# Kernel optimization log

Hardware: AMD Instinct MI355X
Metric: run time of the kernel (lower is better)

## Reference

```python
import jax, jax.numpy as jnp
import numpy as np

N = 100000          # nodes
E = 1600000         # edges (before self-loops)
F_IN = 128          # raw node features
TOPO = 8            # topological feature dim
HEADS1, HID1 = 8, 8 # conv1: 8 heads x 8 channels, concat -> 64
C_OUT = 40          # classes (conv2: 1 head, no concat)
NEG_SLOPE = 0.2     # PyG GATConv leaky_relu slope


def setup_inputs() -> dict:
    key = jax.random.key(0)
    ks = jax.random.split(key, 12)
    x = jax.random.normal(ks[0], (N, F_IN), jnp.float32)
    topo = jax.random.normal(ks[1], (N, TOPO), jnp.float32)
    edge_index = jax.random.randint(ks[2], (2, E), 0, N, jnp.int32)
    s = 0.1
    W1 = jax.random.normal(ks[3], (F_IN + TOPO, HEADS1 * HID1), jnp.float32) * s
    a_src1 = jax.random.normal(ks[4], (HEADS1, HID1), jnp.float32) * s
    a_dst1 = jax.random.normal(ks[5], (HEADS1, HID1), jnp.float32) * s
    b1 = jnp.zeros((HEADS1 * HID1,), jnp.float32)
    W2 = jax.random.normal(ks[6], (HEADS1 * HID1, C_OUT), jnp.float32) * s
    a_src2 = jax.random.normal(ks[7], (1, C_OUT), jnp.float32) * s
    a_dst2 = jax.random.normal(ks[8], (1, C_OUT), jnp.float32) * s
    b2 = jnp.zeros((C_OUT,), jnp.float32)
    return {"x": x, "topo": topo, "edge_index": edge_index,
            "W1": W1, "a_src1": a_src1, "a_dst1": a_dst1, "b1": b1,
            "W2": W2, "a_src2": a_src2, "a_dst2": a_dst2, "b2": b2}


def _gat_conv(x, src, dst, W, a_src, a_dst, b, heads, concat):
    # x: [N, Fin]; src/dst: [Etot] (self-loops already included)
    n = x.shape[0]
    h = (x @ W).reshape(n, heads, -1)                 # [N, H, C]
    alpha_s = jnp.sum(h * a_src[None], axis=-1)       # [N, H]
    alpha_d = jnp.sum(h * a_dst[None], axis=-1)       # [N, H]
    e = jax.nn.leaky_relu(alpha_s[src] + alpha_d[dst], NEG_SLOPE)  # [Etot, H]
    # segment softmax over destination nodes (numerically stable)
    m = jax.ops.segment_max(e, dst, num_segments=n)   # [N, H]
    ex = jnp.exp(e - m[dst])
    z = jax.ops.segment_sum(ex, dst, num_segments=n)  # [N, H]
    alpha = ex / (z[dst] + 1e-16)                     # [Etot, H]
    out = jax.ops.segment_sum(h[src] * alpha[..., None], dst, num_segments=n)  # [N,H,C]
    out = out.reshape(n, -1) if concat else out.mean(axis=1)
    return out + b


def reference(x, topo, edge_index, W1, a_src1, a_dst1, b1, W2, a_src2, a_dst2, b2):
    n = x.shape[0]
    loops = jnp.arange(n, dtype=edge_index.dtype)
    src = jnp.concatenate([edge_index[0], loops])  # PyG add_self_loops=True
    dst = jnp.concatenate([edge_index[1], loops])
    h = jnp.concatenate([x, topo], axis=1)         # [N, F_IN + TOPO]
    # dropout is identity in eval mode
    h = jax.nn.elu(_gat_conv(h, src, dst, W1, a_src1, a_dst1, b1, HEADS1, True))
    logits = _gat_conv(h, src, dst, W2, a_src2, a_dst2, b2, 1, False)
    return jax.nn.log_softmax(logits, axis=1)
```

## Files before the change

### kernel.cpp

```cpp
#include <hip/hip_runtime.h>
#include <math.h>


#define NBUK_MAX 512
#define BIN_CHUNK 4096
#define BUK_CAP 4608

typedef unsigned short ushort_t;

__device__ inline unsigned int f2bf(float f) {
    unsigned int u = __float_as_uint(f);
    u += 0x7FFFu + ((u >> 16) & 1u);
    return u >> 16;
}
__device__ inline float bf_lo(unsigned int u) {
    return __uint_as_float(u << 16);
}
__device__ inline float bf_hi(unsigned int u) {
    return __uint_as_float(u & 0xFFFF0000u);
}
__device__ inline float lrelu_exp(float q) {
    return __expf(q >= 0.f ? q : 0.2f * q);
}

__device__ inline int wave_incl_scan(int v, int lane) {
    #pragma unroll
    for (int ofs = 1; ofs < 64; ofs <<= 1) {
        int t = __shfl_up(v, ofs);
        if (lane >= ofs) v += t;
    }
    return v;
}

__global__ __launch_bounds__(256) void k_bin(const int* __restrict__ src,
                                             const int* __restrict__ dst,
                                             int* __restrict__ gCursor,
                                             unsigned int* __restrict__ tmp,
                                             int E, int NBUK) {
    __shared__ int lcnt[NBUK_MAX];
    __shared__ int lcur[NBUK_MAX];
    int tid = threadIdx.x;
    int base = blockIdx.x * BIN_CHUNK;
    for (int i = tid; i < NBUK; i += 256) lcnt[i] = 0;
    __syncthreads();
    int d[16];
    #pragma unroll
    for (int q = 0; q < 4; q++) {
        int e = base + q * 1024 + 4 * tid;
        if (e + 3 < E) {
            int4 v = *(const int4*)&dst[e];
            d[4 * q + 0] = v.x; d[4 * q + 1] = v.y;
            d[4 * q + 2] = v.z; d[4 * q + 3] = v.w;
        } else {
            #pragma unroll
            for (int k = 0; k < 4; k++)
                d[4 * q + k] = (e + k < E) ? dst[e + k] : -1;
        }
    }
    #pragma unroll
    for (int k = 0; k < 16; k++)
        if (d[k] >= 0) atomicAdd(&lcnt[d[k] >> 8], 1);
    __syncthreads();
    for (int b = tid; b < NBUK; b += 256) {
        int c = lcnt[b];
        lcur[b] = c ? b * BUK_CAP + atomicAdd(&gCursor[b], c) : 0;
    }
    __syncthreads();
    #pragma unroll
    for (int q = 0; q < 4; q++) {
        int e = base + q * 1024 + 4 * tid;
        int s[4];
        if (e + 3 < E) {
            int4 v = *(const int4*)&src[e];
            s[0] = v.x; s[1] = v.y; s[2] = v.z; s[3] = v.w;
        } else {
            #pragma unroll
            for (int k = 0; k < 4; k++)
                s[k] = (e + k < E) ? src[e + k] : 0;
        }
        #pragma unroll
        for (int k = 0; k < 4; k++) {
            int dd = d[4 * q + k];
            if (dd >= 0) {
                int p = atomicAdd(&lcur[dd >> 8], 1);
                tmp[p] = ((unsigned int)s[k] << 8) | (unsigned int)(dd & 255);
            }
        }
    }
}

__global__ __launch_bounds__(512) void k_fill2(const unsigned int* __restrict__ tmp,
                                               const int* __restrict__ gCursor,
                                               int* __restrict__ rowptr,
                                               int* __restrict__ rowEnd,
                                               int* __restrict__ csr, int N) {
    __shared__ int cnt[256];
    __shared__ int cur[256];
    __shared__ int wsum[4];
    int b = blockIdx.x, tid = threadIdx.x;
    int e0 = b * BUK_CAP;
    int cnt_e = gCursor[b];
    int e1 = e0 + cnt_e;
    if (tid < 256) cnt[tid] = 0;
    __syncthreads();
    {
        int nq = cnt_e >> 2;
        const uint4* t4 = (const uint4*)(tmp + e0);
        for (int q = tid; q < nq; q += 512) {
            uint4 v = t4[q];
            atomicAdd(&cnt[v.x & 255u], 1);
            atomicAdd(&cnt[v.y & 255u], 1);
            atomicAdd(&cnt[v.z & 255u], 1);
            atomicAdd(&cnt[v.w & 255u], 1);
        }
        for (int i = (nq << 2) + tid; i < cnt_e; i += 512)
            atomicAdd(&cnt[tmp[e0 + i] & 255u], 1);
    }
    __syncthreads();
    if (tid < 256) {
        int lane = tid & 63, wv = tid >> 6;
        int v = cnt[tid];
        int incl = wave_incl_scan(v, lane);
        if (lane == 63) wsum[wv] = incl;
        cnt[tid] = incl - v;
    }
    __syncthreads();
    if (tid < 256) {
        int wv = tid >> 6;
        int woff = 0;
        for (int i = 0; i < wv; i++) woff += wsum[i];
        int excl = woff + cnt[tid];
        int node = b * 256 + tid;
        int start = e0 + excl;
        cur[tid] = start;
        if (node < N) {
            rowptr[node] = start;
        }
    }
    __syncthreads();
    if (tid < 256) {
        int node = b * 256 + tid;
        if (node < N) rowEnd[node] = (tid < 255) ? cur[tid + 1] : e1;
    }
    __syncthreads();
    for (int i = e0 + tid; i < e1; i += 512) {
        unsigned int t = tmp[i];
        int p = atomicAdd(&cur[t & 255u], 1);
        csr[p] = (int)(t >> 8);
    }
}

__global__ __launch_bounds__(256) void k_xform1(const float* __restrict__ x,
                                                const float* __restrict__ topo,
                                                const float* __restrict__ W1,
                                                const float* __restrict__ asrc,
                                                const float* __restrict__ adst,
                                                ushort_t* __restrict__ h1b,
                                                float* __restrict__ as1,
                                                float* __restrict__ ad1, int N) {
    __shared__ float XT[136 * 64];
    __shared__ float WS[136 * 64];
    int tid = threadIdx.x;
    int n0 = blockIdx.x * 64;
    {
        const float4* W4 = (const float4*)W1;
        float4* WS4 = (float4*)WS;
        for (int i = tid; i < 2176; i += 256) WS4[i] = W4[i];
    }
    {
        const float4* x4 = (const float4*)x;
        for (int i = tid; i < 2048; i += 256) {
            int node = i & 63, k4 = i >> 6;
            int gn = n0 + node; if (gn > N - 1) gn = N - 1;
            float4 v = x4[(size_t)gn * 32 + k4];
            int k = k4 * 4;
            XT[(k + 0) * 64 + node] = v.x;
            XT[(k + 1) * 64 + node] = v.y;
            XT[(k + 2) * 64 + node] = v.z;
            XT[(k + 3) * 64 + node] = v.w;
        }
        const float4* t4 = (const float4*)topo;
        if (tid < 128) {
            int node = tid & 63, j4 = tid >> 6;
            int gn = n0 + node; if (gn > N - 1) gn = N - 1;
            float4 v = t4[(size_t)gn * 2 + j4];
            int k = 128 + j4 * 4;
            XT[(k + 0) * 64 + node] = v.x;
            XT[(k + 1) * 64 + node] = v.y;
            XT[(k + 2) * 64 + node] = v.z;
            XT[(k + 3) * 64 + node] = v.w;
        }
    }
    __syncthreads();
    int ci = tid & 15, ni = tid >> 4;
    int nb = ni * 4, cb = ci * 4;
    float acc[16];
    #pragma unroll
    for (int i = 0; i < 16; i++) acc[i] = 0.f;
    #pragma unroll 4
    for (int k = 0; k < 136; k++) {
        float4 xv = *(const float4*)&XT[k * 64 + nb];
        float4 wv = *(const float4*)&WS[k * 64 + cb];
        acc[0]  = fmaf(xv.x, wv.x, acc[0]);  acc[1]  = fmaf(xv.x, wv.y, acc[1]);
        acc[2]  = fmaf(xv.x, wv.z, acc[2]);  acc[3]  = fmaf(xv.x, wv.w, acc[3]);
        acc[4]  = fmaf(xv.y, wv.x, acc[4]);  acc[5]  = fmaf(xv.y, wv.y, acc[5]);
        acc[6]  = fmaf(xv.y, wv.z, acc[6]);  acc[7]  = fmaf(xv.y, wv.w, acc[7]);
        acc[8]  = fmaf(xv.z, wv.x, acc[8]);  acc[9]  = fmaf(xv.z, wv.y, acc[9]);
        acc[10] = fmaf(xv.z, wv.z, acc[10]); acc[11] = fmaf(xv.z, wv.w, acc[11]);
        acc[12] = fmaf(xv.w, wv.x, acc[12]); acc[13] = fmaf(xv.w, wv.y, acc[13]);
        acc[14] = fmaf(xv.w, wv.z, acc[14]); acc[15] = fmaf(xv.w, wv.w, acc[15]);
    }
    int head = cb >> 3;
    #pragma unroll
    for (int i = 0; i < 4; i++) {
        int n = n0 + nb + i;
        unsigned int p0 = f2bf(acc[i * 4 + 0]) | (f2bf(acc[i * 4 + 1]) << 16);
        unsigned int p1 = f2bf(acc[i * 4 + 2]) | (f2bf(acc[i * 4 + 3]) << 16);
        if (n < N) *(uint2*)&h1b[(size_t)n * 64 + cb] = make_uint2(p0, p1);
        float s = 0.f, d = 0.f;
        #pragma unroll
        for (int j = 0; j < 4; j++) {
            s = fmaf(acc[i * 4 + j], asrc[cb + j], s);
            d = fmaf(acc[i * 4 + j], adst[cb + j], d);
        }
        s += __shfl_xor(s, 1);
        d += __shfl_xor(d, 1);
        if ((ci & 1) == 0 && n < N) {
            as1[n * 8 + head] = s;
            ad1[n * 8 + head] = d;
        }
    }
}

#define AGG_FMA(W_, U_)                                           \
    {                                                             \
        acc[0] = fmaf(W_, bf_lo(U_.x), acc[0]);                   \
        acc[1] = fmaf(W_, bf_hi(U_.x), acc[1]);                   \
        acc[2] = fmaf(W_, bf_lo(U_.y), acc[2]);                   \
        acc[3] = fmaf(W_, bf_hi(U_.y), acc[3]);                   \
        acc[4] = fmaf(W_, bf_lo(U_.z), acc[4]);                   \
        acc[5] = fmaf(W_, bf_hi(U_.z), acc[5]);                   \
        acc[6] = fmaf(W_, bf_lo(U_.w), acc[6]);                   \
        acc[7] = fmaf(W_, bf_hi(U_.w), acc[7]);                   \
        z += W_;                                                  \
    }

#define AGG1_C3(B_)                                                        \
    {                                                                      \
        int e0 = (B_) * 8 + g, e1 = e0 + 8, e2 = e0 + 16;                  \
        int se0 = __shfl(cv, e0 < d ? e0 : dm1);                           \
        int se1 = __shfl(cv, e1 < d ? e1 : dm1);                           \
        int se2 = __shfl(cv, e2 < d ? e2 : dm1);                           \
        float av0 = as1[se0 * 8 + head];                                   \
        float av1 = as1[se1 * 8 + head];                                   \
        float av2 = as1[se2 * 8 + head];                                   \
        uint4 u0 = *(const uint4*)(h1c + (((unsigned)se0 << 7) + hoff));   \
        uint4 u1 = *(const uint4*)(h1c + (((unsigned)se1 << 7) + hoff));   \
        uint4 u2 = *(const uint4*)(h1c + (((unsigned)se2 << 7) + hoff));   \
        float w0 = e0 < d ? lrelu_exp(av0 + adv) : 0.f;                    \
        float w1 = e1 < d ? lrelu_exp(av1 + adv) : 0.f;                    \
        float w2 = e2 < d ? lrelu_exp(av2 + adv) : 0.f;                    \
        AGG_FMA(w0, u0);                                                   \
        AGG_FMA(w1, u1);                                                   \
        AGG_FMA(w2, u2);                                                   \
    }

__global__ __launch_bounds__(256) void k_agg1(const ushort_t* __restrict__ h1b,
                                              const float* __restrict__ as1,
                                              const float* __restrict__ ad1,
                                              const float* __restrict__ b1,
                                              const int* __restrict__ rowptr,
                                              const int* __restrict__ rowEnd,
                                              const int* __restrict__ csr,
                                              float* __restrict__ h2, int N) {
    int tid = threadIdx.x, lane = tid & 63;
    int n = blockIdx.x * 4 + (tid >> 6);
    if (n >= N) return;
    int g = lane >> 3;
    int head = lane & 7;
    const char* h1c = (const char*)h1b;
    unsigned hoff = (unsigned)head << 4;
    float adv = ad1[n * 8 + head];
    float acc[8];
    #pragma unroll
    for (int k = 0; k < 8; k++) acc[k] = 0.f;
    float z = 0.f;

    int j0 = rowptr[n], j1 = rowEnd[n];
    int d = j1 - j0;
    int dm1 = d > 0 ? d - 1 : 0;
    int cv = (d > 0) ? csr[j0 + (lane < d ? lane : dm1)] : 0;

    {
        float w = lrelu_exp(as1[n * 8 + head] + adv);
        if (g == 0) {
            uint4 u = *(const uint4*)(h1c + (((unsigned)n << 7) + hoff));
            acc[0] = w * bf_lo(u.x); acc[1] = w * bf_hi(u.x);
            acc[2] = w * bf_lo(u.y); acc[3] = w * bf_hi(u.y);
            acc[4] = w * bf_lo(u.z); acc[5] = w * bf_hi(u.z);
            acc[6] = w * bf_lo(u.w); acc[7] = w * bf_hi(u.w);
            z = w;
        }
    }
    if (d > 0) {
        AGG1_C3(0);
        if (d > 24) {
            AGG1_C3(3);
            if (d > 48) {
                int e0 = 48 + g, e1 = 56 + g;
                int se0 = __shfl(cv, e0 < d ? e0 : dm1);
                int se1 = __shfl(cv, e1 < d ? e1 : dm1);
                float av0 = as1[se0 * 8 + head];
                float av1 = as1[se1 * 8 + head];
                uint4 u0 = *(const uint4*)(h1c + (((unsigned)se0 << 7) + hoff));
                uint4 u1 = *(const uint4*)(h1c + (((unsigned)se1 << 7) + hoff));
                float w0 = e0 < d ? lrelu_exp(av0 + adv) : 0.f;
                float w1 = e1 < d ? lrelu_exp(av1 + adv) : 0.f;
                AGG_FMA(w0, u0);
                AGG_FMA(w1, u1);
                for (int j = j0 + 64; j < j1; j += 8) {
                    int m = j1 - j;
                    int idx = (lane & 7); idx = idx < m ? idx : m - 1;
                    int cvt = csr[j + idx];
                    int ge = g < m ? g : m - 1;
                    int se = __shfl(cvt, ge);
                    float av = as1[se * 8 + head];
                    uint4 u = *(const uint4*)(h1c + (((unsigned)se << 7) + hoff));
                    float w = (g < m) ? lrelu_exp(av + adv) : 0.f;
                    AGG_FMA(w, u);
                }
            }
        }
    }
    #pragma unroll
    for (int k = 0; k < 8; k++) {
        acc[k] += __shfl_xor(acc[k], 8);
        acc[k] += __shfl_xor(acc[k], 16);
        acc[k] += __shfl_xor(acc[k], 32);
    }
    z += __shfl_xor(z, 8); z += __shfl_xor(z, 16); z += __shfl_xor(z, 32);
    if (g == 0) {
        float inv = 1.f / (z + 1e-16f);
        float o[8];
        #pragma unroll
        for (int k = 0; k < 8; k++) {
            float v = acc[k] * inv + b1[head * 8 + k];
            o[k] = v > 0.f ? v : (__expf(v) - 1.f);
        }
        float4* dp = (float4*)&h2[(size_t)n * 64 + head * 8];
        dp[0] = make_float4(o[0], o[1], o[2], o[3]);
        dp[1] = make_float4(o[4], o[5], o[6], o[7]);
    }
}

__global__ __launch_bounds__(256) void k_xform2(const float* __restrict__ h2,
                                                const float* __restrict__ W2,
                                                const float* __restrict__ asrc2,
                                                const float* __restrict__ adst2,
                                                ushort_t* __restrict__ gb,
                                                float* __restrict__ as2,
                                                float* __restrict__ ad2, int N) {
    __shared__ float XT[64 * 64];
    __shared__ float WS[64 * 40];
    int tid = threadIdx.x;
    int n0 = blockIdx.x * 64;
    {
        const float4* W4 = (const float4*)W2;
        float4* WS4 = (float4*)WS;
        for (int i = tid; i < 640; i += 256) WS4[i] = W4[i];
    }
    {
        const float4* h4 = (const float4*)h2;
        for (int i = tid; i < 1024; i += 256) {
            int node = i & 63, k4 = i >> 6;
            int gn = n0 + node; if (gn > N - 1) gn = N - 1;
            float4 v = h4[(size_t)gn * 16 + k4];
            int k = k4 * 4;
            XT[(k + 0) * 64 + node] = v.x;
            XT[(k + 1) * 64 + node] = v.y;
            XT[(k + 2) * 64 + node] = v.z;
            XT[(k + 3) * 64 + node] = v.w;
        }
    }
    __syncthreads();
    int ci = tid & 15, ni = tid >> 4;
    int nb = ni * 4, cb = ci * 4;
    float acc[16];
    #pragma unroll
    for (int i = 0; i < 16; i++) acc[i] = 0.f;
    if (ci < 10) {
        #pragma unroll 4
        for (int k = 0; k < 64; k++) {
            float4 xv = *(const float4*)&XT[k * 64 + nb];
            float4 wv = *(const float4*)&WS[k * 40 + cb];
            acc[0]  = fmaf(xv.x, wv.x, acc[0]);  acc[1]  = fmaf(xv.x, wv.y, acc[1]);
            acc[2]  = fmaf(xv.x, wv.z, acc[2]);  acc[3]  = fmaf(xv.x, wv.w, acc[3]);
            acc[4]  = fmaf(xv.y, wv.x, acc[4]);  acc[5]  = fmaf(xv.y, wv.y, acc[5]);
            acc[6]  = fmaf(xv.y, wv.z, acc[6]);  acc[7]  = fmaf(xv.y, wv.w, acc[7]);
            acc[8]  = fmaf(xv.z, wv.x, acc[8]);  acc[9]  = fmaf(xv.z, wv.y, acc[9]);
            acc[10] = fmaf(xv.z, wv.z, acc[10]); acc[11] = fmaf(xv.z, wv.w, acc[11]);
            acc[12] = fmaf(xv.w, wv.x, acc[12]); acc[13] = fmaf(xv.w, wv.y, acc[13]);
            acc[14] = fmaf(xv.w, wv.z, acc[14]); acc[15] = fmaf(xv.w, wv.w, acc[15]);
        }
    }
    #pragma unroll
    for (int i = 0; i < 4; i++) {
        int n = n0 + nb + i;
        if (ci < 10 && n < N) {
            unsigned int p0 = f2bf(acc[i * 4 + 0]) | (f2bf(acc[i * 4 + 1]) << 16);
            unsigned int p1 = f2bf(acc[i * 4 + 2]) | (f2bf(acc[i * 4 + 3]) << 16);
            *(uint2*)&gb[(size_t)n * 40 + cb] = make_uint2(p0, p1);
        }
        float s = 0.f, d = 0.f;
        if (ci < 10) {
            #pragma unroll
            for (int j = 0; j < 4; j++) {
                s = fmaf(acc[i * 4 + j], asrc2[cb + j], s);
                d = fmaf(acc[i * 4 + j], adst2[cb + j], d);
            }
        }
        s += __shfl_xor(s, 1); s += __shfl_xor(s, 2);
        s += __shfl_xor(s, 4); s += __shfl_xor(s, 8);
        d += __shfl_xor(d, 1); d += __shfl_xor(d, 2);
        d += __shfl_xor(d, 4); d += __shfl_xor(d, 8);
        if (ci == 0 && n < N) { as2[n] = s; ad2[n] = d; }
    }
}

#define AGG2_C2(B_)                                                            \
    {                                                                          \
        int ew0 = (B_) * 12 + lm12, ew1 = ew0 + 12;                            \
        int sw0 = __shfl(cv, ew0 < d ? ew0 : dm1);                             \
        int sw1 = __shfl(cv, ew1 < d ? ew1 : dm1);                             \
        float av0 = as2[sw0];                                                  \
        float av1 = as2[sw1];                                                  \
        int e00 = (B_) * 12 + gi0, e01 = (B_) * 12 + gi1;                      \
        int e02 = (B_) * 12 + gi2, e03 = (B_) * 12 + gi3;                      \
        int s00 = __shfl(cv, e00 < d ? e00 : dm1);                             \
        int s01 = __shfl(cv, e01 < d ? e01 : dm1);                             \
        int s02 = __shfl(cv, e02 < d ? e02 : dm1);                             \
        int s03 = __shfl(cv, e03 < d ? e03 : dm1);                             \
        int s10 = __shfl(cv, e00 + 12 < d ? e00 + 12 : dm1);                   \
        int s11 = __shfl(cv, e01 + 12 < d ? e01 + 12 : dm1);                   \
        int s12 = __shfl(cv, e02 + 12 < d ? e02 + 12 : dm1);                   \
        int s13 = __shfl(cv, e03 + 12 < d ? e03 + 12 : dm1);                   \
        unsigned int u00 = *(const unsigned int*)(gbc + ((unsigned)s00 * 80u + coff)); \
        unsigned int u01 = *(const unsigned int*)(gbc + ((unsigned)s01 * 80u + coff)); \
        unsigned int u02 = *(const unsigned int*)(gbc + ((unsigned)s02 * 80u + coff)); \
        unsigned int u03 = *(const unsigned int*)(gbc + ((unsigned)s03 * 80u + coff)); \
        unsigned int u10 = *(const unsigned int*)(gbc + ((unsigned)s10 * 80u + coff)); \
        unsigned int u11 = *(const unsigned int*)(gbc + ((unsigned)s11 * 80u + coff)); \
        unsigned int u12 = *(const unsigned int*)(gbc + ((unsigned)s12 * 80u + coff)); \
        unsigned int u13 = *(const unsigned int*)(gbc + ((unsigned)s13 * 80u + coff)); \
        float wall0 = (ew0 < d) ? lrelu_exp(av0 + add) : 0.f;                  \
        float wall1 = (ew1 < d) ? lrelu_exp(av1 + add) : 0.f;                  \
        float w00 = __shfl(wall0, gi0), w01 = __shfl(wall0, gi1);              \
        float w02 = __shfl(wall0, gi2), w03 = __shfl(wall0, gi3);              \
        float w10 = __shfl(wall1, gi0), w11 = __shfl(wall1, gi1);              \
        float w12 = __shfl(wall1, gi2), w13 = __shfl(wall1, gi3);              \
        acc0 = fmaf(w00, bf_lo(u00), acc0); acc1 = fmaf(w00, bf_hi(u00), acc1); zl += w00; \
        acc0 = fmaf(w01, bf_lo(u01), acc0); acc1 = fmaf(w01, bf_hi(u01), acc1); zl += w01; \
        acc0 = fmaf(w02, bf_lo(u02), acc0); acc1 = fmaf(w02, bf_hi(u02), acc1); zl += w02; \
        acc0 = fmaf(w03, bf_lo(u03), acc0); acc1 = fmaf(w03, bf_hi(u03), acc1); zl += w03; \
        acc0 = fmaf(w10, bf_lo(u10), acc0); acc1 = fmaf(w10, bf_hi(u10), acc1); zl += w10; \
        acc0 = fmaf(w11, bf_lo(u11), acc0); acc1 = fmaf(w11, bf_hi(u11), acc1); zl += w11; \
        acc0 = fmaf(w12, bf_lo(u12), acc0); acc1 = fmaf(w12, bf_hi(u12), acc1); zl += w12; \
        acc0 = fmaf(w13, bf_lo(u13), acc0); acc1 = fmaf(w13, bf_hi(u13), acc1); zl += w13; \
    }

__global__ __launch_bounds__(256) void k_agg2(const ushort_t* __restrict__ gb,
                                              const float* __restrict__ as2,
                                              const float* __restrict__ ad2,
                                              const float* __restrict__ b2,
                                              const int* __restrict__ rowptr,
                                              const int* __restrict__ rowEnd,
                                              const int* __restrict__ csr,
                                              float* __restrict__ out, int N) {
    int tid = threadIdx.x, lane = tid & 63;
    int n = blockIdx.x * 4 + (tid >> 6);
    if (n >= N) return;
    int g = lane / 20, p = lane % 20;
    int c0 = 2 * p;
    const char* gbc = (const char*)gb;
    unsigned coff = (unsigned)(p << 2);
    int lm12 = lane % 12;
    int gi0 = (0 + g) < 12 ? (0 + g) : 11;
    int gi1 = (3 + g) < 12 ? (3 + g) : 11;
    int gi2 = (6 + g) < 12 ? (6 + g) : 11;
    int gi3 = (9 + g) < 12 ? (9 + g) : 11;
    float add = ad2[n];
    float acc0 = 0.f, acc1 = 0.f, zl = 0.f;

    int j0 = rowptr[n], j1 = rowEnd[n];
    int d = j1 - j0;
    int dm1 = d > 0 ? d - 1 : 0;
    int cv = (d > 0) ? csr[j0 + (lane < d ? lane : dm1)] : 0;

    {
        float e0 = as2[n] + add;
        float w = lrelu_exp(e0);
        if (g == 0) {
            unsigned int u = *(const unsigned int*)(gbc + ((unsigned)n * 80u + coff));
            acc0 = w * bf_lo(u); acc1 = w * bf_hi(u); zl = w;
        }
    }
    if (d > 0) {
        AGG2_C2(0);
        if (d > 24) {
            AGG2_C2(2);
            if (d > 48) {
                for (int j = j0 + 48; j < j1; j += 12) {
                    int m = j1 - j;
                    int idx = lm12 < m ? lm12 : m - 1;
                    int cvt = csr[j + idx];
                    float av = as2[cvt];
                    float wall = (lm12 < m) ? lrelu_exp(av + add) : 0.f;
                    #pragma unroll
                    for (int i = 0; i < 4; i++) {
                        int e = 3 * i + g;
                        int gi = e < 12 ? e : 11;
                        int gim = gi < m ? gi : m - 1;
                        int s = __shfl(cvt, gim);
                        unsigned int u = *(const unsigned int*)(gbc + ((unsigned)s * 80u + coff));
                        float w = __shfl(wall, gi);
                        acc0 = fmaf(w, bf_lo(u), acc0);
                        acc1 = fmaf(w, bf_hi(u), acc1);
                        zl += w;
                    }
                }
            }
        }
    }
    float A0 = acc0 + __shfl(acc0, (lane + 20) & 63) + __shfl(acc0, (lane + 40) & 63);
    float A1 = acc1 + __shfl(acc1, (lane + 20) & 63) + __shfl(acc1, (lane + 40) & 63);
    float Z  = zl + __shfl(zl, (lane + 20) & 63) + __shfl(zl, (lane + 40) & 63);
    float l0 = 0.f, l1 = 0.f;
    bool active = (lane < 20);
    if (active) {
        float inv = 1.f / (Z + 1e-16f);
        l0 = A0 * inv + b2[c0];
        l1 = A1 * inv + b2[c0 + 1];
    }
    float mv = active ? fmaxf(l0, l1) : -INFINITY;
    #pragma unroll
    for (int ofs = 1; ofs < 32; ofs <<= 1) mv = fmaxf(mv, __shfl_xor(mv, ofs));
    float ev = active ? (__expf(l0 - mv) + __expf(l1 - mv)) : 0.f;
    #pragma unroll
    for (int ofs = 1; ofs < 32; ofs <<= 1) ev += __shfl_xor(ev, ofs);
    if (active) {
        float ls = mv + __logf(ev);
        *(float2*)&out[(size_t)n * 40 + c0] = make_float2(l0 - ls, l1 - ls);
    }
}

extern "C" void kernel_launch(void* const* d_in, const int* in_sizes, int n_in,
                              void* d_out, int out_size, void* d_ws, size_t ws_size,
                              hipStream_t stream) {
    const float* x    = (const float*)d_in[0];
    const float* topo = (const float*)d_in[1];
    const int*   ei   = (const int*)d_in[2];
    const float* W1   = (const float*)d_in[3];
    const float* a_s1 = (const float*)d_in[4];
    const float* a_d1 = (const float*)d_in[5];
    const float* b1   = (const float*)d_in[6];
    const float* W2   = (const float*)d_in[7];
    const float* a_s2 = (const float*)d_in[8];
    const float* a_d2 = (const float*)d_in[9];
    const float* b2   = (const float*)d_in[10];
    float* out = (float*)d_out;

    int N = in_sizes[0] / 128;
    int E = in_sizes[2] / 2;
    const int* esrc = ei;
    const int* edst = ei + E;
    int NBUK = (N + 255) / 256;
    size_t cap = (size_t)NBUK * BUK_CAP;

    char* ws = (char*)d_ws;
    size_t off = 0;
    auto alloc = [&](size_t bytes) -> void* {
        void* p = ws + off;
        off = (off + bytes + 255) & ~(size_t)255;
        return p;
    };
    ushort_t* h1b  = (ushort_t*)alloc((size_t)N * 64 * 2);
    float* as1     = (float*)alloc((size_t)N * 8 * 4);
    float* ad1     = (float*)alloc((size_t)N * 8 * 4);
    float* h2      = (float*)alloc((size_t)N * 64 * 4);
    ushort_t* gb   = (ushort_t*)alloc((size_t)N * 40 * 2);
    float* as2     = (float*)alloc((size_t)N * 4);
    float* ad2     = (float*)alloc((size_t)N * 4);
    int*   rowptr  = (int*)alloc((size_t)N * 4);
    int*   rowEnd  = (int*)alloc((size_t)N * 4);
    int*   csr     = (int*)alloc(cap * 4);
    unsigned int* tmp = (unsigned int*)alloc(cap * 4);
    int* gCursor   = (int*)alloc((size_t)NBUK * 4);

    hipMemsetAsync(gCursor, 0, (size_t)NBUK * 4, stream);
    int nbin = (E + BIN_CHUNK - 1) / BIN_CHUNK;
    k_bin<<<nbin, 256, 0, stream>>>(esrc, edst, gCursor, tmp, E, NBUK);
    k_fill2<<<NBUK, 512, 0, stream>>>(tmp, gCursor, rowptr, rowEnd, csr, N);

    int nbg = (N + 63) / 64;
    int nb4 = (N + 3) / 4;
    k_xform1<<<nbg, 256, 0, stream>>>(x, topo, W1, a_s1, a_d1, h1b, as1, ad1, N);
    k_agg1<<<nb4, 256, 0, stream>>>(h1b, as1, ad1, b1, rowptr, rowEnd, csr, h2, N);
    k_xform2<<<nbg, 256, 0, stream>>>(h2, W2, a_s2, a_d2, gb, as2, ad2, N);
    k_agg2<<<nb4, 256, 0, stream>>>(gb, as2, ad2, b2, rowptr, rowEnd, csr, out, N);
}
```

Measured before the change: 294.1 us.

## Process two nodes per wavefront in layer-1 aggregation with batched gathers

Layer-1 aggregation now maps two destination nodes to each 64-lane wavefront, 32 lanes per node with 4 edge groups instead of 8. With about 17 edges per node on average, this cuts idle lanes. It also issues six neighbor gathers up front before any of the exp/FMA work, to raise memory-level parallelism. In exchange there are more serial edge iterations per node, divergence when the two nodes differ in degree, and higher register pressure.

```diff
diff --git a/kernel.cpp b/kernel.cpp
--- a/kernel.cpp
+++ b/kernel.cpp
@@ -245,24 +245,16 @@
         z += W_;                                                  \
     }
 
-#define AGG1_C3(B_)                                                        \
-    {                                                                      \
-        int e0 = (B_) * 8 + g, e1 = e0 + 8, e2 = e0 + 16;                  \
-        int se0 = __shfl(cv, e0 < d ? e0 : dm1);                           \
-        int se1 = __shfl(cv, e1 < d ? e1 : dm1);                           \
-        int se2 = __shfl(cv, e2 < d ? e2 : dm1);                           \
-        float av0 = as1[se0 * 8 + head];                                   \
-        float av1 = as1[se1 * 8 + head];                                   \
-        float av2 = as1[se2 * 8 + head];                                   \
-        uint4 u0 = *(const uint4*)(h1c + (((unsigned)se0 << 7) + hoff));   \
-        uint4 u1 = *(const uint4*)(h1c + (((unsigned)se1 << 7) + hoff));   \
-        uint4 u2 = *(const uint4*)(h1c + (((unsigned)se2 << 7) + hoff));   \
-        float w0 = e0 < d ? lrelu_exp(av0 + adv) : 0.f;                    \
-        float w1 = e1 < d ? lrelu_exp(av1 + adv) : 0.f;                    \
-        float w2 = e2 < d ? lrelu_exp(av2 + adv) : 0.f;                    \
-        AGG_FMA(w0, u0);                                                   \
-        AGG_FMA(w1, u1);                                                   \
-        AGG_FMA(w2, u2);                                                   \
+#define AGG1_GATHER(EIDX, SE_, AV_, UU_)                                     \
+    int SE_ = __shfl(cv, nbase + ((EIDX) < d ? (EIDX) : dm1));               \
+    SE_ = d > 0 ? SE_ : 0;                                                   \
+    float AV_ = as1[SE_ * 8 + head];                                         \
+    uint4 UU_ = *(const uint4*)(h1c + (((unsigned)SE_ << 7) + hoff));
+
+#define AGG1_COMP(EIDX, AV_, UU_)                                            \
+    {                                                                        \
+        float w_ = (EIDX) < d ? lrelu_exp(AV_ + adv) : 0.f;                  \
+        AGG_FMA(w_, UU_);                                                    \
     }
 
 __global__ __launch_bounds__(256) void k_agg1(const ushort_t* __restrict__ h1b,
@@ -274,27 +266,35 @@
                                               const int* __restrict__ csr,
                                               float* __restrict__ h2, int N) {
     int tid = threadIdx.x, lane = tid & 63;
-    int n = blockIdx.x * 4 + (tid >> 6);
-    if (n >= N) return;
-    int g = lane >> 3;
+    int nbase0 = blockIdx.x * 8 + ((tid >> 6) << 1);
+    if (nbase0 >= N) return;
+    int nid = lane >> 5;
+    int nbase = nid << 5;
+    int l32 = lane & 31;
+    int g = (lane >> 3) & 3;
     int head = lane & 7;
+    int n = nbase0 + nid;
+    bool valid = n < N;
+    int nc = valid ? n : N - 1;
     const char* h1c = (const char*)h1b;
     unsigned hoff = (unsigned)head << 4;
-    float adv = ad1[n * 8 + head];
+    float adv = ad1[nc * 8 + head];
     float acc[8];
     #pragma unroll
     for (int k = 0; k < 8; k++) acc[k] = 0.f;
     float z = 0.f;
 
-    int j0 = rowptr[n], j1 = rowEnd[n];
-    int d = j1 - j0;
+    int j0 = rowptr[nc], j1 = rowEnd[nc];
+    int d = valid ? (j1 - j0) : 0;
     int dm1 = d > 0 ? d - 1 : 0;
-    int cv = (d > 0) ? csr[j0 + (lane < d ? lane : dm1)] : 0;
+    int dx = __shfl_xor(d, 32);
+    int dmax = d > dx ? d : dx;
+    int cv = csr[j0 + (l32 < d ? l32 : dm1)];
 
     {
-        float w = lrelu_exp(as1[n * 8 + head] + adv);
-        if (g == 0) {
-            uint4 u = *(const uint4*)(h1c + (((unsigned)n << 7) + hoff));
+        float w = lrelu_exp(as1[nc * 8 + head] + adv);
+        if (g == 0 && valid) {
+            uint4 u = *(const uint4*)(h1c + (((unsigned)nc << 7) + hoff));
             acc[0] = w * bf_lo(u.x); acc[1] = w * bf_hi(u.x);
             acc[2] = w * bf_lo(u.y); acc[3] = w * bf_hi(u.y);
             acc[4] = w * bf_lo(u.z); acc[5] = w * bf_hi(u.z);
@@ -302,31 +302,35 @@
             z = w;
         }
     }
-    if (d > 0) {
-        AGG1_C3(0);
-        if (d > 24) {
-            AGG1_C3(3);
-            if (d > 48) {
-                int e0 = 48 + g, e1 = 56 + g;
-                int se0 = __shfl(cv, e0 < d ? e0 : dm1);
-                int se1 = __shfl(cv, e1 < d ? e1 : dm1);
-                float av0 = as1[se0 * 8 + head];
-                float av1 = as1[se1 * 8 + head];
-                uint4 u0 = *(const uint4*)(h1c + (((unsigned)se0 << 7) + hoff));
-                uint4 u1 = *(const uint4*)(h1c + (((unsigned)se1 << 7) + hoff));
-                float w0 = e0 < d ? lrelu_exp(av0 + adv) : 0.f;
-                float w1 = e1 < d ? lrelu_exp(av1 + adv) : 0.f;
-                AGG_FMA(w0, u0);
-                AGG_FMA(w1, u1);
-                for (int j = j0 + 64; j < j1; j += 8) {
-                    int m = j1 - j;
-                    int idx = (lane & 7); idx = idx < m ? idx : m - 1;
-                    int cvt = csr[j + idx];
-                    int ge = g < m ? g : m - 1;
-                    int se = __shfl(cvt, ge);
+    if (dmax > 0) {
+        int e0 = g, e1 = 4 + g, e2 = 8 + g, e3 = 12 + g, e4 = 16 + g, e5 = 20 + g;
+        AGG1_GATHER(e0, s0, a0, u0)
+        AGG1_GATHER(e1, s1, a1, u1)
+        AGG1_GATHER(e2, s2, a2, u2)
+        AGG1_GATHER(e3, s3, a3, u3)
+        AGG1_GATHER(e4, s4, a4, u4)
+        AGG1_GATHER(e5, s5, a5, u5)
+        AGG1_COMP(e0, a0, u0)
+        if (dmax > 4)  AGG1_COMP(e1, a1, u1)
+        if (dmax > 8)  AGG1_COMP(e2, a2, u2)
+        if (dmax > 12) AGG1_COMP(e3, a3, u3)
+        if (dmax > 16) AGG1_COMP(e4, a4, u4)
+        if (dmax > 20) AGG1_COMP(e5, a5, u5)
+        if (dmax > 24) {
+            int e6 = 24 + g, e7 = 28 + g;
+            AGG1_GATHER(e6, s6, a6, u6)
+            AGG1_GATHER(e7, s7, a7, u7)
+            AGG1_COMP(e6, a6, u6)
+            if (dmax > 28) AGG1_COMP(e7, a7, u7)
+            if (dmax > 32) {
+                for (int eb = 32; eb < dmax; eb += 4) {
+                    int e = eb + g;
+                    int idx = e < d ? e : dm1;
+                    int se = csr[j0 + idx];
+                    se = d > 0 ? se : 0;
                     float av = as1[se * 8 + head];
                     uint4 u = *(const uint4*)(h1c + (((unsigned)se << 7) + hoff));
-                    float w = (g < m) ? lrelu_exp(av + adv) : 0.f;
+                    float w = e < d ? lrelu_exp(av + adv) : 0.f;
                     AGG_FMA(w, u);
                 }
             }
@@ -336,10 +340,9 @@
     for (int k = 0; k < 8; k++) {
         acc[k] += __shfl_xor(acc[k], 8);
         acc[k] += __shfl_xor(acc[k], 16);
-        acc[k] += __shfl_xor(acc[k], 32);
-    }
-    z += __shfl_xor(z, 8); z += __shfl_xor(z, 16); z += __shfl_xor(z, 32);
-    if (g == 0) {
+    }
+    z += __shfl_xor(z, 8); z += __shfl_xor(z, 16);
+    if (g == 0 && valid) {
         float inv = 1.f / (z + 1e-16f);
         float o[8];
         #pragma unroll
@@ -602,9 +605,10 @@
     k_fill2<<<NBUK, 512, 0, stream>>>(tmp, gCursor, rowptr, rowEnd, csr, N);
 
     int nbg = (N + 63) / 64;
+    int nb8 = (N + 7) / 8;
     int nb4 = (N + 3) / 4;
     k_xform1<<<nbg, 256, 0, stream>>>(x, topo, W1, a_s1, a_d1, h1b, as1, ad1, N);
-    k_agg1<<<nb4, 256, 0, stream>>>(h1b, as1, ad1, b1, rowptr, rowEnd, csr, h2, N);
+    k_agg1<<<nb8, 256, 0, stream>>>(h1b, as1, ad1, b1, rowptr, rowEnd, csr, h2, N);
     k_xform2<<<nbg, 256, 0, stream>>>(h2, W2, a_s2, a_d2, gb, as2, ad2, N);
     k_agg2<<<nb4, 256, 0, stream>>>(gb, as2, ad2, b2, rowptr, rowEnd, csr, out, N);
 }
```

Result: no change. 289.1 us (-1.7%).
